# Kernel tuning notes

Hardware: AMD Instinct MI355X
Metric: run time of the kernel (lower is better)

Reference implementation:

```python
import jax, jax.numpy as jnp
import numpy as np

P = 4   # patch_size
H = 8   # num_heads


def setup_inputs() -> dict:
    key = jax.random.key(0)
    k0, k1, k2 = jax.random.split(key, 3)
    B, C, R = 8, 8, 64
    E = C * P ** 3  # 512
    s = 1.0 / np.sqrt(E)
    x = jax.random.normal(k0, (B, C, R, R, R), jnp.float32)
    in_proj_w = jax.random.normal(k1, (3 * E, E), jnp.float32) * s
    in_proj_b = jnp.zeros((3 * E,), jnp.float32)
    out_proj_w = jax.random.normal(k2, (E, E), jnp.float32) * s
    out_proj_b = jnp.zeros((E,), jnp.float32)
    return {"x": x, "in_proj_w": in_proj_w, "in_proj_b": in_proj_b,
            "out_proj_w": out_proj_w, "out_proj_b": out_proj_b}


def reference(x, in_proj_w, in_proj_b, out_proj_w, out_proj_b):
    B, C, Rx, Ry, Rz = x.shape
    p = P
    nx, ny, nz = Rx // p, Ry // p, Rz // p
    N = nx * ny * nz
    E = C * p ** 3
    dh = E // H

    # cyclic shift: move last patch to front == roll by +p on each spatial axis
    x = jnp.roll(x, (p, p, p), axis=(2, 3, 4))

    # window partition: (B,C,nx,p,ny,p,nz,p) -> (B, N, C*p^3), matching
    # unfold + flatten + permute + flatten of the torch code
    xw = (x.reshape(B, C, nx, p, ny, p, nz, p)
           .transpose(0, 2, 4, 6, 1, 3, 5, 7)
           .reshape(B, N, E))

    # nn.MultiheadAttention with batch_first=False: seq dim = B, batch dim = N
    qkv = jnp.einsum('bne,fe->bnf', xw, in_proj_w) + in_proj_b  # (B, N, 3E)
    q, k, v = jnp.split(qkv, 3, axis=-1)
    q = q.reshape(B, N, H, dh)
    k = k.reshape(B, N, H, dh)
    v = v.reshape(B, N, H, dh)
    scale = 1.0 / np.sqrt(dh)
    # attention over the B (sequence) axis, independently per window n and head h
    att = jax.nn.softmax(jnp.einsum('inhd,jnhd->nhij', q * scale, k), axis=-1)
    o = jnp.einsum('nhij,jnhd->inhd', att, v).reshape(B, N, E)
    o = jnp.einsum('bne,fe->bnf', o, out_proj_w) + out_proj_b  # (B, N, E)

    # torch reassembly via the cat-of-permute loops interleaves windows:
    # out[b, c, px*nx + ix, py*ny + iy, pz*nz + iz] = y[b, ix, iy, iz, c, px, py, pz]
    y = (o.reshape(B, nx, ny, nz, C, p, p, p)
          .transpose(0, 4, 5, 1, 6, 2, 7, 3)
          .reshape(B, C, Rx, Ry, Rz))

    # reverse cyclic shift: roll by -p on each spatial axis
    y = jnp.roll(y, (-p, -p, -p), axis=(2, 3, 4))
    return y
```

## Files before the change

kernel.cpp:

```cpp
#include <hip/hip_runtime.h>

typedef unsigned short u16;
typedef unsigned int u32;
typedef __bf16 bf16x8 __attribute__((ext_vector_type(8)));
typedef float f32x16 __attribute__((ext_vector_type(16)));

__device__ __forceinline__ u16 f2bf(float f) {
  u32 u = __builtin_bit_cast(u32, f);
  u = (u + 0x7FFFu + ((u >> 16) & 1u)) >> 16;
  return (u16)u;
}
__device__ __forceinline__ float bf2f(u16 h) {
  u32 u = ((u32)h) << 16;
  return __builtin_bit_cast(float, u);
}

#define GLD16(gp, lp) __builtin_amdgcn_global_load_lds( \
    (const __attribute__((address_space(1))) u32*)(const void*)(gp), \
    (__attribute__((address_space(3))) u32*)(void*)(lp), 16, 0, 0)
#define SBAR() __builtin_amdgcn_s_barrier()
#define SCHED0() __builtin_amdgcn_sched_barrier(0)

__global__ __launch_bounds__(256) void cast_both(const float* __restrict__ w_in,
                                                 u16* __restrict__ wq,
                                                 const float* __restrict__ w_out,
                                                 u16* __restrict__ wo) {
  int i = blockIdx.x * 256 + threadIdx.x;
  const float* src = w_in; u16* dst = wq; int idx = i;
  if (i >= 196608) { src = w_out; dst = wo; idx = i - 196608; }
  float4 v = *(const float4*)(src + (size_t)idx * 4);
  ushort4 u;
  u.x = f2bf(v.x); u.y = f2bf(v.y); u.z = f2bf(v.z); u.w = f2bf(v.w);
  *(ushort4*)(dst + (size_t)idx * 4) = u;
}

__global__ __launch_bounds__(256) void permute_in(const float* __restrict__ x,
                                                  u16* __restrict__ xw) {
  __shared__ float lds[128 * 64];
  int t = threadIdx.x;
  int bx = blockIdx.x;
  int b = blockIdx.y;
  int jx = bx >> 4, jy = bx & 15;
#pragma unroll
  for (int it = 0; it < 8; ++it) {
    int idx = t + it * 256;
    int row = idx >> 4, z4 = idx & 15;
    int c = row >> 4, qx = (row >> 2) & 3, qy = row & 3;
    int X = (jx * 4 + qx + 60) & 63;
    int Y = (jy * 4 + qy + 60) & 63;
    float4 v = *(const float4*)(x + ((((size_t)(b * 8 + c) * 64 + X) * 64 + Y) * 64 + z4 * 4));
    *(float4*)(lds + row * 64 + ((z4 ^ (row & 7)) << 2)) = v;
  }
  __syncthreads();
#pragma unroll
  for (int it = 0; it < 8; ++it) {
    int idx = t + it * 256;
    int jz = idx >> 7, r = idx & 127;
    int z4r = (jz + 15) & 15;
    float4 v = *(const float4*)(lds + r * 64 + ((z4r ^ (r & 7)) << 2));
    int nw = jx * 256 + jy * 16 + jz;
    ushort4 u;
    u.x = f2bf(v.x); u.y = f2bf(v.y); u.z = f2bf(v.z); u.w = f2bf(v.w);
    *(ushort4*)(xw + (size_t)(nw * 8 + b) * 512 + r * 4) = u;
  }
}

__global__ __launch_bounds__(256, 3) void gemm_qkv_attn(const u16* __restrict__ A,
                                                        const u16* __restrict__ W,
                                                        const float* __restrict__ bias,
                                                        u16* __restrict__ O) {
  __shared__ u16 smem[20480];
  u16* As = smem;
  u16* Bs = smem + 8192;
  float* ctf = (float*)smem;

  int cpx = gridDim.x >> 3;
  int wg = (blockIdx.x & 7) * cpx + (blockIdx.x >> 3);
  int mbc = wg >> 3, h = wg & 7;
  int m0 = mbc * 128;

  int tid = threadIdx.x;
  int wv = tid >> 6, l = tid & 63;
  int wr = wv >> 1, wc = wv & 1;
  int l31 = l & 31, g = l >> 5;

  int kch = ((l & 3) ^ ((l >> 3) & 3)) * 8;
  const u16* pa[2]; int dA[2];
#pragma unroll
  for (int i = 0; i < 2; ++i) {
    int slot = wv * 128 + i * 64 + l;
    int row = slot >> 2;
    pa[i] = A + (size_t)(m0 + row) * 512 + kch;
    dA[i] = (wv * 128 + i * 64) * 8;
  }
  const u16* pb[3]; int dB[3];
#pragma unroll
  for (int i = 0; i < 3; ++i) {
    int slot = wv * 192 + i * 64 + l;
    int row = slot >> 2;
    int grow = (row >> 6) * 512 + h * 64 + (row & 63);
    pb[i] = W + (size_t)grow * 512 + kch;
    dB[i] = (wv * 192 + i * 64) * 8;
  }

  int abase[2], bbase[3];
#pragma unroll
  for (int m = 0; m < 2; ++m) abase[m] = (wr * 64 + m * 32 + l31) * 32;
#pragma unroll
  for (int n = 0; n < 3; ++n) bbase[n] = (wc * 96 + n * 32 + l31) * 32;
  int rsw = (l31 >> 1) & 3;

  f32x16 acc[2][3] = {};

  GLD16(pa[0], As + dA[0]); GLD16(pa[1], As + dA[1]);
  GLD16(pb[0], Bs + dB[0]); GLD16(pb[1], Bs + dB[1]); GLD16(pb[2], Bs + dB[2]);
  asm volatile("s_waitcnt vmcnt(0)" ::: "memory");
  SCHED0(); SBAR(); SCHED0();

  for (int t = 0; t < 16; ++t) {
    const u16* AsT = As + (t & 1) * 4096;
    const u16* BsT = Bs + (t & 1) * 6144;
    u16* Ad = As + ((t + 1) & 1) * 4096;
    u16* Bd = Bs + ((t + 1) & 1) * 6144;
    int nx = (t + 1) * 32;
    bool st = t < 15;
#pragma unroll
    for (int s = 0; s < 2; ++s) {
      int cofs = ((((s << 1) | g) ^ rsw)) << 3;
      bf16x8 af[2], bf[3];
      af[0] = *(const bf16x8*)(AsT + abase[0] + cofs);
      af[1] = *(const bf16x8*)(AsT + abase[1] + cofs);
      bf[0] = *(const bf16x8*)(BsT + bbase[0] + cofs);
      bf[1] = *(const bf16x8*)(BsT + bbase[1] + cofs);
      bf[2] = *(const bf16x8*)(BsT + bbase[2] + cofs);
      if (s == 0 && st) { GLD16(pa[0] + nx, Ad + dA[0]); GLD16(pa[1] + nx, Ad + dA[1]); }
      if (s == 1 && st) {
        GLD16(pb[0] + nx, Bd + dB[0]); GLD16(pb[1] + nx, Bd + dB[1]);
        GLD16(pb[2] + nx, Bd + dB[2]);
      }
      SCHED0();
      __builtin_amdgcn_s_setprio(1);
#pragma unroll
      for (int m = 0; m < 2; ++m)
#pragma unroll
        for (int n = 0; n < 3; ++n)
          acc[m][n] = __builtin_amdgcn_mfma_f32_32x32x16_bf16(bf[n], af[m], acc[m][n], 0, 0, 0);
      __builtin_amdgcn_s_setprio(0);
      SCHED0();
    }
    asm volatile("s_waitcnt vmcnt(0)" ::: "memory");
    SCHED0(); SBAR(); SCHED0();
  }

#pragma unroll
  for (int c = 0; c < 4; ++c) {
    if ((c >> 1) == wr) {
      const int m = c & 1;
#pragma unroll
      for (int n = 0; n < 3; ++n)
#pragma unroll
        for (int q = 0; q < 4; ++q) {
          int col0 = wc * 96 + n * 32 + q * 8 + g * 4;
          int gcol = ((col0 >> 6) << 9) + (h << 6) + (col0 & 63);
          float4 bv = *(const float4*)(bias + gcol);
          float4 stv;
          stv.x = acc[m][n][q * 4 + 0] + bv.x;
          stv.y = acc[m][n][q * 4 + 1] + bv.y;
          stv.z = acc[m][n][q * 4 + 2] + bv.z;
          stv.w = acc[m][n][q * 4 + 3] + bv.w;
          *(float4*)(ctf + l31 * 204 + col0) = stv;
        }
    }
    __syncthreads();
    {
      int qi = l >> 3, j = l & 7;
      const float* qr = ctf + (wv * 8 + qi) * 204;
      const float* kr = ctf + (wv * 8 + j) * 204 + 64;
      float sc = 0.f;
#pragma unroll
      for (int d = 0; d < 16; ++d) {
        float4 qv = *(const float4*)(qr + d * 4);
        float4 kv = *(const float4*)(kr + d * 4);
        sc += qv.x * kv.x + qv.y * kv.y + qv.z * kv.z + qv.w * kv.w;
      }
      sc *= 0.125f;
      float mx = sc;
      mx = fmaxf(mx, __shfl_xor(mx, 1));
      mx = fmaxf(mx, __shfl_xor(mx, 2));
      mx = fmaxf(mx, __shfl_xor(mx, 4));
      float p = __expf(sc - mx);
      float sum = p;
      sum += __shfl_xor(sum, 1);
      sum += __shfl_xor(sum, 2);
      sum += __shfl_xor(sum, 4);
      p /= sum;
      float pr[8];
      int lb = l & 56;
#pragma unroll
      for (int jj = 0; jj < 8; ++jj) pr[jj] = __shfl(p, lb + jj);
      float ov[8] = {};
#pragma unroll
      for (int jj = 0; jj < 8; ++jj) {
        const float* vr = ctf + (wv * 8 + jj) * 204 + 128 + j * 8;
        float4 va = *(const float4*)(vr);
        float4 vb = *(const float4*)(vr + 4);
        float pj = pr[jj];
        ov[0] += pj * va.x; ov[1] += pj * va.y; ov[2] += pj * va.z; ov[3] += pj * va.w;
        ov[4] += pj * vb.x; ov[5] += pj * vb.y; ov[6] += pj * vb.z; ov[7] += pj * vb.w;
      }
      ushort4 r0, r1;
      r0.x = f2bf(ov[0]); r0.y = f2bf(ov[1]); r0.z = f2bf(ov[2]); r0.w = f2bf(ov[3]);
      r1.x = f2bf(ov[4]); r1.y = f2bf(ov[5]); r1.z = f2bf(ov[6]); r1.w = f2bf(ov[7]);
      u16* dst = O + (size_t)(m0 + c * 32 + wv * 8 + qi) * 512 + h * 64 + j * 8;
      *(ushort4*)dst = r0;
      *(ushort4*)(dst + 4) = r1;
    }
    __syncthreads();
  }
}

__global__ __launch_bounds__(512, 4) void gemm_out(const u16* __restrict__ A,
                                                   const u16* __restrict__ Wt,
                                                   const float* __restrict__ bias,
                                                   u16* __restrict__ C) {
  __shared__ u16 smem[24576];
  u16* As = smem;
  u16* Bs = smem + 16384;

  int cpx = gridDim.x >> 3;
  int wg = (blockIdx.x & 7) * cpx + (blockIdx.x >> 3);
  int mb = wg >> 2, nb = wg & 3;
  int m0 = mb * 256, n0 = nb * 128;

  int tid = threadIdx.x;
  int wv = tid >> 6, l = tid & 63;
  int wr = wv >> 1, wc = wv & 1;
  int l31 = l & 31, g = l >> 5;

  int kch = ((l & 3) ^ ((l >> 3) & 3)) * 8;
  const u16* pa[2]; int dA[2];
#pragma unroll
  for (int i = 0; i < 2; ++i) {
    int slot = wv * 128 + i * 64 + l;
    int row = slot >> 2;
    pa[i] = A + (size_t)(m0 + row) * 512 + kch;
    dA[i] = (wv * 128 + i * 64) * 8;
  }
  int slotB = wv * 64 + l;
  int rowB = slotB >> 2;
  const u16* pb = Wt + (size_t)(n0 + rowB) * 512 + kch;
  int dB = (wv * 64) * 8;

  int abase[2], bbase[2];
#pragma unroll
  for (int m = 0; m < 2; ++m) abase[m] = (wr * 64 + m * 32 + l31) * 32;
#pragma unroll
  for (int n = 0; n < 2; ++n) bbase[n] = (wc * 64 + n * 32 + l31) * 32;
  int rsw = (l31 >> 1) & 3;

  f32x16 acc[2][2] = {};

  GLD16(pa[0], As + dA[0]); GLD16(pa[1], As + dA[1]);
  GLD16(pb, Bs + dB);
  asm volatile("s_waitcnt vmcnt(0)" ::: "memory");
  SCHED0(); SBAR(); SCHED0();

  for (int t = 0; t < 16; ++t) {
    const u16* AsT = As + (t & 1) * 8192;
    const u16* BsT = Bs + (t & 1) * 4096;
    u16* Ad = As + ((t + 1) & 1) * 8192;
    u16* Bd = Bs + ((t + 1) & 1) * 4096;
    int nx = (t + 1) * 32;
    bool st = t < 15;
#pragma unroll
    for (int s = 0; s < 2; ++s) {
      int cofs = ((((s << 1) | g) ^ rsw)) << 3;
      bf16x8 af[2], bf[2];
      af[0] = *(const bf16x8*)(AsT + abase[0] + cofs);
      af[1] = *(const bf16x8*)(AsT + abase[1] + cofs);
      bf[0] = *(const bf16x8*)(BsT + bbase[0] + cofs);
      bf[1] = *(const bf16x8*)(BsT + bbase[1] + cofs);
      if (s == 0 && st) { GLD16(pa[0] + nx, Ad + dA[0]); GLD16(pa[1] + nx, Ad + dA[1]); }
      if (s == 1 && st) { GLD16(pb + nx, Bd + dB); }
      SCHED0();
      __builtin_amdgcn_s_setprio(1);
#pragma unroll
      for (int m = 0; m < 2; ++m)
#pragma unroll
        for (int n = 0; n < 2; ++n)
          acc[m][n] = __builtin_amdgcn_mfma_f32_32x32x16_bf16(bf[n], af[m], acc[m][n], 0, 0, 0);
      __builtin_amdgcn_s_setprio(0);
      SCHED0();
    }
    asm volatile("s_waitcnt vmcnt(0)" ::: "memory");
    SCHED0(); SBAR(); SCHED0();
  }

#pragma unroll
  for (int m = 0; m < 2; ++m) {
    size_t row = (size_t)(m0 + wr * 64 + m * 32 + l31);
#pragma unroll
    for (int n = 0; n < 2; ++n)
#pragma unroll
      for (int q = 0; q < 4; ++q) {
        int col0 = n0 + wc * 64 + n * 32 + q * 8 + g * 4;
        float4 bv = *(const float4*)(bias + col0);
        ushort4 uu;
        uu.x = f2bf(acc[m][n][q * 4 + 0] + bv.x);
        uu.y = f2bf(acc[m][n][q * 4 + 1] + bv.y);
        uu.z = f2bf(acc[m][n][q * 4 + 2] + bv.z);
        uu.w = f2bf(acc[m][n][q * 4 + 3] + bv.w);
        *(ushort4*)(C + row * 512 + col0) = uu;
      }
  }
}

__global__ __launch_bounds__(256) void permute_out(const u16* __restrict__ o2,
                                                   float* __restrict__ out) {
  __shared__ float lds[16 * 516];
  int t = threadIdx.x;
  int bx = blockIdx.x;
  int b = blockIdx.y;
  int ix = bx >> 4, iy = bx & 15;
  int n0 = ix * 256 + iy * 16;
#pragma unroll
  for (int it = 0; it < 8; ++it) {
    int idx = t + it * 256;
    int iz = idx >> 7, fq = idx & 127;
    ushort4 u = *(const ushort4*)(o2 + ((size_t)((n0 + iz) * 8 + b) * 512 + fq * 4));
    float4 v;
    v.x = bf2f(u.x); v.y = bf2f(u.y); v.z = bf2f(u.z); v.w = bf2f(u.w);
    *(float4*)(lds + iz * 516 + fq * 4) = v;
  }
  __syncthreads();
#pragma unroll
  for (int it = 0; it < 8; ++it) {
    int idx = t + it * 256;
    int fidx = idx >> 4, w4 = idx & 15;
    int c = fidx >> 4, px = (fidx >> 2) & 3, py = fidx & 3;
    int W0 = (w4 * 4 + 4) & 63;
    int pz = W0 >> 4, iz0 = W0 & 15;
    int fa = fidx * 4 + pz;
    float4 v;
    v.x = lds[(iz0 + 0) * 516 + fa];
    v.y = lds[(iz0 + 1) * 516 + fa];
    v.z = lds[(iz0 + 2) * 516 + fa];
    v.w = lds[(iz0 + 3) * 516 + fa];
    int uu = (px * 16 + ix + 60) & 63;
    int vv = (py * 16 + iy + 60) & 63;
    *(float4*)(out + ((((size_t)(b * 8 + c) * 64 + uu) * 64 + vv) * 64 + w4 * 4)) = v;
  }
}

extern "C" void kernel_launch(void* const* d_in, const int* in_sizes, int n_in,
                              void* d_out, int out_size, void* d_ws, size_t ws_size,
                              hipStream_t stream) {
  const float* x     = (const float*)d_in[0];
  const float* w_in  = (const float*)d_in[1];
  const float* b_in  = (const float*)d_in[2];
  const float* w_out = (const float*)d_in[3];
  const float* b_out = (const float*)d_in[4];
  float* out = (float*)d_out;

  char* ws = (char*)d_ws;
  u16* wq  = (u16*)(ws);
  u16* wo  = (u16*)(ws + 1572864);
  u16* xw2 = (u16*)(ws + 2097152);
  u16* o   = (u16*)(ws + 35651584);
  u16* o2  = (u16*)(ws + 69206016);

  cast_both<<<1024, 256, 0, stream>>>(w_in, wq, w_out, wo);
  permute_in<<<dim3(256, 8), 256, 0, stream>>>(x, xw2);
  gemm_qkv_attn<<<2048, 256, 0, stream>>>(xw2, wq, b_in, o);
  gemm_out<<<512, 512, 0, stream>>>(o, wo, b_out, o2);
  permute_out<<<dim3(256, 8), 256, 0, stream>>>(o2, out);
}
```

Before: 157.7 us.

## Deepen QKV GEMM pipeline to four LDS stages and swizzle epilogue LDS

Turns the QKV+attention GEMM's double-buffered LDS pipeline into a 4-stage ring with 3 tiles in flight, using partial vmcnt waits so global loads overlap several MFMA iterations. LDS doubles, so launch bounds drop from 3 to 2 blocks per CU, trading occupancy for latency hiding. The fp32 epilogue staging buffer also gets an XOR swizzle on columns to cut LDS bank conflicts in the attention reads.

Measured after the change: 158.0 us. Within noise of the previous version (+0.2%).

```diff
diff --git a/kernel.cpp b/kernel.cpp
--- a/kernel.cpp
+++ b/kernel.cpp
@@ -65,13 +65,13 @@
   }
 }
 
-__global__ __launch_bounds__(256, 3) void gemm_qkv_attn(const u16* __restrict__ A,
+__global__ __launch_bounds__(256, 2) void gemm_qkv_attn(const u16* __restrict__ A,
                                                         const u16* __restrict__ W,
                                                         const float* __restrict__ bias,
                                                         u16* __restrict__ O) {
-  __shared__ u16 smem[20480];
+  __shared__ u16 smem[40960];
   u16* As = smem;
-  u16* Bs = smem + 8192;
+  u16* Bs = smem + 16384;
   float* ctf = (float*)smem;
 
   int cpx = gridDim.x >> 3;
@@ -112,18 +112,25 @@
 
   f32x16 acc[2][3] = {};
 
-  GLD16(pa[0], As + dA[0]); GLD16(pa[1], As + dA[1]);
-  GLD16(pb[0], Bs + dB[0]); GLD16(pb[1], Bs + dB[1]); GLD16(pb[2], Bs + dB[2]);
-  asm volatile("s_waitcnt vmcnt(0)" ::: "memory");
+#pragma unroll
+  for (int ts = 0; ts < 3; ++ts) {
+    int kadd = ts * 32;
+    GLD16(pa[0] + kadd, As + ts * 4096 + dA[0]);
+    GLD16(pa[1] + kadd, As + ts * 4096 + dA[1]);
+    GLD16(pb[0] + kadd, Bs + ts * 6144 + dB[0]);
+    GLD16(pb[1] + kadd, Bs + ts * 6144 + dB[1]);
+    GLD16(pb[2] + kadd, Bs + ts * 6144 + dB[2]);
+  }
+  asm volatile("s_waitcnt vmcnt(10)" ::: "memory");
   SCHED0(); SBAR(); SCHED0();
 
   for (int t = 0; t < 16; ++t) {
-    const u16* AsT = As + (t & 1) * 4096;
-    const u16* BsT = Bs + (t & 1) * 6144;
-    u16* Ad = As + ((t + 1) & 1) * 4096;
-    u16* Bd = Bs + ((t + 1) & 1) * 6144;
-    int nx = (t + 1) * 32;
-    bool st = t < 15;
+    const u16* AsT = As + (t & 3) * 4096;
+    const u16* BsT = Bs + (t & 3) * 6144;
+    u16* Ad = As + ((t + 3) & 3) * 4096;
+    u16* Bd = Bs + ((t + 3) & 3) * 6144;
+    int nx = (t + 3) * 32;
+    bool st = t + 3 < 16;
 #pragma unroll
     for (int s = 0; s < 2; ++s) {
       int cofs = ((((s << 1) | g) ^ rsw)) << 3;
@@ -148,14 +155,24 @@
       __builtin_amdgcn_s_setprio(0);
       SCHED0();
     }
-    asm volatile("s_waitcnt vmcnt(0)" ::: "memory");
-    SCHED0(); SBAR(); SCHED0();
-  }
+    if (t <= 12) {
+      asm volatile("s_waitcnt vmcnt(10)" ::: "memory");
+    } else if (t == 13) {
+      asm volatile("s_waitcnt vmcnt(5)" ::: "memory");
+    } else if (t == 14) {
+      asm volatile("s_waitcnt vmcnt(0)" ::: "memory");
+    }
+    SCHED0();
+    if (t < 15) { SBAR(); SCHED0(); }
+  }
+
+  __syncthreads();
 
 #pragma unroll
   for (int c = 0; c < 4; ++c) {
     if ((c >> 1) == wr) {
       const int m = c & 1;
+      int skey = ((l31 >> 3) & 3) << 2;
 #pragma unroll
       for (int n = 0; n < 3; ++n)
 #pragma unroll
@@ -168,19 +185,20 @@
           stv.y = acc[m][n][q * 4 + 1] + bv.y;
           stv.z = acc[m][n][q * 4 + 2] + bv.z;
           stv.w = acc[m][n][q * 4 + 3] + bv.w;
-          *(float4*)(ctf + l31 * 204 + col0) = stv;
+          *(float4*)(ctf + l31 * 204 + (col0 ^ skey)) = stv;
         }
     }
     __syncthreads();
     {
       int qi = l >> 3, j = l & 7;
+      int K4 = wv << 2;
       const float* qr = ctf + (wv * 8 + qi) * 204;
-      const float* kr = ctf + (wv * 8 + j) * 204 + 64;
+      const float* kr = ctf + (wv * 8 + j) * 204;
       float sc = 0.f;
 #pragma unroll
       for (int d = 0; d < 16; ++d) {
-        float4 qv = *(const float4*)(qr + d * 4);
-        float4 kv = *(const float4*)(kr + d * 4);
+        float4 qv = *(const float4*)(qr + ((d * 4) ^ K4));
+        float4 kv = *(const float4*)(kr + ((64 + d * 4) ^ K4));
         sc += qv.x * kv.x + qv.y * kv.y + qv.z * kv.z + qv.w * kv.w;
       }
       sc *= 0.125f;
@@ -201,9 +219,10 @@
       float ov[8] = {};
 #pragma unroll
       for (int jj = 0; jj < 8; ++jj) {
-        const float* vr = ctf + (wv * 8 + jj) * 204 + 128 + j * 8;
-        float4 va = *(const float4*)(vr);
-        float4 vb = *(const float4*)(vr + 4);
+        const float* vr = ctf + (wv * 8 + jj) * 204;
+        int b0 = 128 + j * 8;
+        float4 va = *(const float4*)(vr + (b0 ^ K4));
+        float4 vb = *(const float4*)(vr + ((b0 + 4) ^ K4));
         float pj = pr[jj];
         ov[0] += pj * va.x; ov[1] += pj * va.y; ov[2] += pj * va.z; ov[3] += pj * va.w;
         ov[4] += pj * vb.x; ov[5] += pj * vb.y; ov[6] += pj * vb.z; ov[7] += pj * vb.w;
```
